# Performance work log

Hardware: AMD Instinct MI355X
Metric: run time of the kernel (lower is better)

Reference implementation:

```python
import jax, jax.numpy as jnp
from jax import lax
import numpy as np

B, MAX_FRAME, CAPLEN = 64, 40, 20
H, E, V = 512, 512, 32000


def setup_inputs() -> dict:
    key = jax.random.key(0)
    ks = jax.random.split(key, 9)
    s = 0.02
    return {
        "feature": jax.random.normal(ks[0], (B, MAX_FRAME + CAPLEN, H), dtype=jnp.float32),
        "captions": jax.random.randint(ks[1], (B, CAPLEN), 0, V),
        "embedding": jax.random.normal(ks[2], (V, E), dtype=jnp.float32) * s,
        "W_ih": jax.random.normal(ks[3], (4 * H, E + H), dtype=jnp.float32) * s,
        "W_hh": jax.random.normal(ks[4], (4 * H, H), dtype=jnp.float32) * s,
        "b_ih": jax.random.normal(ks[5], (4 * H,), dtype=jnp.float32) * s,
        "b_hh": jax.random.normal(ks[6], (4 * H,), dtype=jnp.float32) * s,
        "W_lin": jax.random.normal(ks[7], (V, H), dtype=jnp.float32) * s,
        "b_lin": jax.random.normal(ks[8], (V,), dtype=jnp.float32) * s,
    }


def _lstm_scan(xs, W_ih, W_hh, b, h0, c0):
    """xs: [T, B, D]; PyTorch gate order i, f, g, o."""
    def step(carry, x):
        h, c = carry
        gates = x @ W_ih.T + h @ W_hh.T + b  # [B, 4H]
        i, f, g, o = jnp.split(gates, 4, axis=-1)
        c = jax.nn.sigmoid(f) * c + jax.nn.sigmoid(i) * jnp.tanh(g)
        h = jax.nn.sigmoid(o) * jnp.tanh(c)
        return (h, c), h
    _, hs = lax.scan(step, (h0, c0), xs)
    return hs  # [T, B, H]


def reference(feature, captions, embedding, W_ih, W_hh, b_ih, b_hh, W_lin, b_lin):
    batch = feature.shape[0]
    caplen = captions.shape[1]
    max_frame = feature.shape[1] - caplen
    hdim = W_hh.shape[1]
    edim = embedding.shape[1]

    emb = embedding[captions]  # [B, caplen, E]
    # encoding phase: pad token (zeros) concat frame feature
    pad = jnp.zeros((batch, max_frame, edim), feature.dtype)
    enc_x = jnp.concatenate([pad, feature[:, :max_frame, :]], axis=2)  # [B, mf, E+H]
    # decoding phase: embedded word concat frame feature
    dec_x = jnp.concatenate([emb, feature[:, max_frame:, :]], axis=2)  # [B, caplen, E+H]
    xs = jnp.concatenate([enc_x, dec_x], axis=1).transpose(1, 0, 2)  # [T, B, E+H]

    h0 = jnp.zeros((batch, hdim), feature.dtype)
    c0 = jnp.zeros((batch, hdim), feature.dtype)
    hs = _lstm_scan(xs, W_ih, W_hh, b_ih + b_hh, h0, c0)  # [T, B, H]

    dec_h = hs[max_frame:].transpose(1, 0, 2)  # [B, caplen, H]
    logits = dec_h @ W_lin.T + b_lin  # [B, caplen, V]
    logits = logits[:, :-1, :]  # drop last step, as in original
    return logits.reshape(batch * (caplen - 1), -1)
```

## Files before the change

kernel.cpp:

```cpp
#include <hip/hip_runtime.h>
#include <hip/hip_bf16.h>


typedef short bf16x8 __attribute__((ext_vector_type(8)));
typedef float f32x4 __attribute__((ext_vector_type(4)));

__device__ inline short f2bf(float f) {
    unsigned u = __float_as_uint(f);
    unsigned r = (u + 0x7fffu + ((u >> 16) & 1u)) >> 16;
    return (short)r;
}
__device__ inline int4 ld8_f32_to_bf16(const float* __restrict__ g) {
    float4 a = *(const float4*)g;
    float4 b = *(const float4*)(g + 4);
    union { short s[8]; int4 v; } u;
    u.s[0] = f2bf(a.x); u.s[1] = f2bf(a.y); u.s[2] = f2bf(a.z); u.s[3] = f2bf(a.w);
    u.s[4] = f2bf(b.x); u.s[5] = f2bf(b.y); u.s[6] = f2bf(b.z); u.s[7] = f2bf(b.w);
    return u.v;
}
__device__ inline float sigf(float x) { return 1.0f / (1.0f + expf(-x)); }

__device__ inline float sig_fast(float x) {
    return __builtin_amdgcn_rcpf(1.0f + __expf(-x));
}
__device__ inline float tanh_fast(float x) {
    return 1.0f - 2.0f * __builtin_amdgcn_rcpf(1.0f + __expf(2.0f * x));
}

__device__ inline void gload_lds16(const void* g, void* l) {
    __builtin_amdgcn_global_load_lds(
        (const __attribute__((address_space(1))) void*)g,
        (__attribute__((address_space(3))) void*)l, 16, 0, 0);
}

__global__ __launch_bounds__(256) void gemm_xproj(
    const float* __restrict__ feature,
    const int*   __restrict__ captions,
    const float* __restrict__ embedding,
    const float* __restrict__ W_ih,
    const float* __restrict__ b_ih,
    const float* __restrict__ b_hh,
    float* __restrict__ Xp)
{
    __shared__ __align__(16) short Al[128 * 72];
    __shared__ __align__(16) short Bl[128 * 72];
    const int tid  = threadIdx.x;
    const int wave = tid >> 6, lane = tid & 63;
    const int quad = lane >> 4, l16 = lane & 15;
    const int m0 = blockIdx.y * 128;
    const int n0 = blockIdx.x * 128;
    const int wm = (wave >> 1) * 64, wn = (wave & 1) * 64;
    const int sr = tid >> 3;
    const int sc = (tid & 7) * 8;

    f32x4 acc[4][4] = {};

    for (int k0 = 0; k0 < 1024; k0 += 64) {
        const int j = k0 + sc;
#pragma unroll
        for (int p = 0; p < 4; ++p) {
            int r = sr + p * 32;
            int row = m0 + r;
            int t = row >> 6, b = row & 63;
            int4 val;
            if (j < 512) {
                if (t >= 40) {
                    int tok = captions[b * 20 + (t - 40)];
                    val = ld8_f32_to_bf16(&embedding[(size_t)tok * 512 + j]);
                } else {
                    val = make_int4(0, 0, 0, 0);
                }
            } else {
                val = ld8_f32_to_bf16(&feature[(size_t)(b * 60 + t) * 512 + (j - 512)]);
            }
            *(int4*)&Al[r * 72 + sc] = val;
            *(int4*)&Bl[r * 72 + sc] = ld8_f32_to_bf16(&W_ih[(size_t)(n0 + r) * 1024 + j]);
        }
        __syncthreads();
#pragma unroll
        for (int kk = 0; kk < 64; kk += 32) {
            bf16x8 af[4], bg[4];
#pragma unroll
            for (int i = 0; i < 4; ++i)
                af[i] = *(const bf16x8*)&Al[(wm + i * 16 + l16) * 72 + kk + quad * 8];
#pragma unroll
            for (int jj = 0; jj < 4; ++jj)
                bg[jj] = *(const bf16x8*)&Bl[(wn + jj * 16 + l16) * 72 + kk + quad * 8];
#pragma unroll
            for (int i = 0; i < 4; ++i)
#pragma unroll
                for (int jj = 0; jj < 4; ++jj)
                    acc[i][jj] = __builtin_amdgcn_mfma_f32_16x16x32_bf16(
                        af[i], bg[jj], acc[i][jj], 0, 0, 0);
        }
        __syncthreads();
    }

#pragma unroll
    for (int jj = 0; jj < 4; ++jj) {
        int n = n0 + wn + jj * 16 + l16;
        float bv = b_ih[n] + b_hh[n];
#pragma unroll
        for (int i = 0; i < 4; ++i) {
            int mbase = m0 + wm + i * 16 + quad * 4;
#pragma unroll
            for (int r = 0; r < 4; ++r)
                Xp[(size_t)(mbase + r) * 2048 + n] = acc[i][jj][r] + bv;
        }
    }
}

__global__ __launch_bounds__(256) void cvt_bf16(
    const float* __restrict__ src, short* __restrict__ dst, int n8)
{
    int i = blockIdx.x * 256 + threadIdx.x;
    if (i < n8)
        *(int4*)&dst[(size_t)i * 8] = ld8_f32_to_bf16(&src[(size_t)i * 8]);
}

template <bool BF16B>
__global__ __launch_bounds__(256) void gemm_out(
    const short* __restrict__ A,
    const void*  __restrict__ Wv,
    const float* __restrict__ bias,
    float* __restrict__ C,
    int M, int N, int K)
{
    __shared__ __align__(16) short Al[128 * 72];
    __shared__ __align__(16) short Bl[128 * 72];
    const int tid  = threadIdx.x;
    const int wave = tid >> 6, lane = tid & 63;
    const int quad = lane >> 4, l16 = lane & 15;
    const int m0 = blockIdx.y * 128;
    const int n0 = blockIdx.x * 128;
    const int wm = (wave >> 1) * 64, wn = (wave & 1) * 64;
    const int sr = tid >> 3;
    const int sc = (tid & 7) * 8;

    f32x4 acc[4][4] = {};

    for (int k0 = 0; k0 < K; k0 += 64) {
        if (BF16B) {
            const char* Ab = (const char*)A;
            const char* Wb = (const char*)Wv;
            char* AlB = (char*)Al;
            char* BlB = (char*)Bl;
#pragma unroll
            for (int p = 0; p < 4; ++p) {
                int row = p * 32 + wave * 8 + (lane >> 3);
                int ss  = ((lane & 7) ^ (row & 7)) << 4;
                int am  = m0 + row; am = (am < M) ? am : (M - 1);
                gload_lds16(Ab + (size_t)am * 1024 + k0 * 2 + ss,
                            AlB + p * 4096 + wave * 1024);
                gload_lds16(Wb + (size_t)(n0 + row) * 1024 + k0 * 2 + ss,
                            BlB + p * 4096 + wave * 1024);
            }
        } else {
#pragma unroll
            for (int p = 0; p < 4; ++p) {
                int r = sr + p * 32;
                int am = m0 + r;
                am = (am < M) ? am : (M - 1);
                *(int4*)&Al[r * 72 + sc] = *(const int4*)&A[(size_t)am * K + k0 + sc];
                *(int4*)&Bl[r * 72 + sc] =
                    ld8_f32_to_bf16(&((const float*)Wv)[(size_t)(n0 + r) * K + k0 + sc]);
            }
        }
        __syncthreads();
#pragma unroll
        for (int kk = 0; kk < 64; kk += 32) {
            bf16x8 af[4], bg[4];
            if (BF16B) {
                const int s_ = (kk >> 3) + quad;
#pragma unroll
                for (int i = 0; i < 4; ++i) {
                    int rw = wm + i * 16 + l16;
                    af[i] = *(const bf16x8*)&Al[rw * 64 + ((s_ ^ (rw & 7)) << 3)];
                }
#pragma unroll
                for (int jj = 0; jj < 4; ++jj) {
                    int rw = wn + jj * 16 + l16;
                    bg[jj] = *(const bf16x8*)&Bl[rw * 64 + ((s_ ^ (rw & 7)) << 3)];
                }
            } else {
#pragma unroll
                for (int i = 0; i < 4; ++i)
                    af[i] = *(const bf16x8*)&Al[(wm + i * 16 + l16) * 72 + kk + quad * 8];
#pragma unroll
                for (int jj = 0; jj < 4; ++jj)
                    bg[jj] = *(const bf16x8*)&Bl[(wn + jj * 16 + l16) * 72 + kk + quad * 8];
            }
#pragma unroll
            for (int i = 0; i < 4; ++i)
#pragma unroll
                for (int jj = 0; jj < 4; ++jj)
                    acc[i][jj] = __builtin_amdgcn_mfma_f32_16x16x32_bf16(
                        af[i], bg[jj], acc[i][jj], 0, 0, 0);
        }
        __syncthreads();
    }

#pragma unroll
    for (int jj = 0; jj < 4; ++jj) {
        int n = n0 + wn + jj * 16 + l16;
        float bv = bias[n];
#pragma unroll
        for (int i = 0; i < 4; ++i) {
            int mbase = m0 + wm + i * 16 + quad * 4;
#pragma unroll
            for (int r = 0; r < 4; ++r) {
                int m = mbase + r;
                if (m < M)
                    C[(size_t)m * N + n] = acc[i][jj][r] + bv;
            }
        }
    }
}

#define LSTM_BLOCKS 32

__global__ __launch_bounds__(256, 1) void lstm_persist(
    const float* __restrict__ Xp,
    const float* __restrict__ W_hh,
    unsigned long long* __restrict__ hbuf,
    unsigned long long* __restrict__ dec_h,
    unsigned* __restrict__ flags)
{
    __shared__ __align__(16) short Wl[64 * 512];
    __shared__ __align__(16) short Ht[4][16][16];
    const int tid  = threadIdx.x;
    const int wave = tid >> 6, lane = tid & 63;
    const int quad = lane >> 4, l16 = lane & 15;
    const int nb = blockIdx.x * 16;
    const int swz = (l16 & 7) << 3;

#pragma unroll
    for (int it = 0; it < 16; ++it) {
        int rr = (tid >> 6) + it * 4;
        int k  = (tid & 63) * 8;
        int s = rr >> 4, col = rr & 15;
        *(int4*)&Wl[(rr * 512 + k) ^ ((rr & 7) << 3)] =
            ld8_f32_to_bf16(&W_hh[(size_t)(s * 512 + nb + col) * 512 + k]);
    }
    float creg[4] = {0.f, 0.f, 0.f, 0.f};

    const int n = nb + l16;
    float xg[4][4];
#pragma unroll
    for (int r = 0; r < 4; ++r) {
        const float* xr = Xp + (size_t)(wave * 16 + quad * 4 + r) * 2048;
        xg[r][0] = xr[n];
        xg[r][1] = xr[512 + n];
        xg[r][2] = xr[1024 + n];
        xg[r][3] = xr[1536 + n];
    }
    __syncthreads();

    for (int t = 0; t < 59; ++t) {
        f32x4 acc[4] = {};
        if (t > 0) {
            const unsigned long long* hrow =
                hbuf + ((size_t)((t & 1) ^ 1) << 13)
                     + (size_t)(wave * 16 + l16) * 128 + quad * 2;
            union { unsigned long long q[2]; bf16x8 v; } hu[16];
#pragma unroll
            for (int kk = 0; kk < 16; ++kk) {
                hu[kk].q[0] = __hip_atomic_load(&hrow[kk * 8],
                                 __ATOMIC_RELAXED, __HIP_MEMORY_SCOPE_AGENT);
                hu[kk].q[1] = __hip_atomic_load(&hrow[kk * 8 + 1],
                                 __ATOMIC_RELAXED, __HIP_MEMORY_SCOPE_AGENT);
            }
            __builtin_amdgcn_sched_barrier(0);
#pragma unroll
            for (int kk = 0; kk < 16; ++kk) {
#pragma unroll
                for (int s = 0; s < 4; ++s) {
                    bf16x8 bg = *(const bf16x8*)
                        &Wl[((s * 16 + l16) * 512 + kk * 32 + quad * 8) ^ swz];
                    acc[s] = __builtin_amdgcn_mfma_f32_16x16x32_bf16(hu[kk].v, bg, acc[s], 0, 0, 0);
                }
            }
        }
#pragma unroll
        for (int r = 0; r < 4; ++r) {
            float iv = acc[0][r] + xg[r][0];
            float fv = acc[1][r] + xg[r][1];
            float gv = acc[2][r] + xg[r][2];
            float ov = acc[3][r] + xg[r][3];
            float cn = sig_fast(fv) * creg[r] + sig_fast(iv) * tanh_fast(gv);
            float hn = sig_fast(ov) * tanh_fast(cn);
            creg[r] = cn;
            Ht[wave][quad * 4 + r][l16] = f2bf(hn);
        }
        asm volatile("s_waitcnt lgkmcnt(0)" ::: "memory");
        unsigned long long* hout64 = hbuf + ((size_t)(t & 1) << 13);
        {
            int row = lane >> 2, qp = lane & 3;
            unsigned long long v = *(const unsigned long long*)&Ht[wave][row][qp * 4];
            int m = wave * 16 + row;
            __hip_atomic_store(&hout64[m * 128 + (nb >> 2) + qp], v,
                               __ATOMIC_RELAXED, __HIP_MEMORY_SCOPE_AGENT);
            if (t >= 40)
                dec_h[(size_t)(m * 19 + (t - 40)) * 128 + (nb >> 2) + qp] = v;
        }
        if (t < 58) {
            float xn_[4][4];
            const float* xt = Xp + (size_t)(t + 1) * 131072;
#pragma unroll
            for (int r = 0; r < 4; ++r) {
                const float* xr = xt + (size_t)(wave * 16 + quad * 4 + r) * 2048;
                xn_[r][0] = xr[n];
                xn_[r][1] = xr[512 + n];
                xn_[r][2] = xr[1024 + n];
                xn_[r][3] = xr[1536 + n];
            }
            __syncthreads();
            if (tid == 0)
                __hip_atomic_store(&flags[blockIdx.x], (unsigned)(t + 1),
                                   __ATOMIC_RELAXED, __HIP_MEMORY_SCOPE_AGENT);
            if (tid < LSTM_BLOCKS) {
                int guard = 0;
                while (__hip_atomic_load(&flags[tid], __ATOMIC_RELAXED,
                                         __HIP_MEMORY_SCOPE_AGENT) < (unsigned)(t + 1)
                       && guard < (1 << 16)) {
                    __builtin_amdgcn_s_sleep(1);
                    ++guard;
                }
            }
            __syncthreads();
#pragma unroll
            for (int r = 0; r < 4; ++r)
#pragma unroll
                for (int g = 0; g < 4; ++g)
                    xg[r][g] = xn_[r][g];
        }
    }
}

extern "C" void kernel_launch(void* const* d_in, const int* in_sizes, int n_in,
                              void* d_out, int out_size, void* d_ws, size_t ws_size,
                              hipStream_t stream)
{
    (void)in_sizes; (void)n_in; (void)out_size;
    const float* feature   = (const float*)d_in[0];
    const int*   captions  = (const int*)d_in[1];
    const float* embedding = (const float*)d_in[2];
    const float* W_ih      = (const float*)d_in[3];
    const float* W_hh      = (const float*)d_in[4];
    const float* b_ih      = (const float*)d_in[5];
    const float* b_hh      = (const float*)d_in[6];
    const float* W_lin     = (const float*)d_in[7];
    const float* b_lin     = (const float*)d_in[8];
    float* out = (float*)d_out;

    char* ws = (char*)d_ws;
    unsigned long long* hbuf = (unsigned long long*)(ws);
    short*    dech = (short*)(ws + 131072);
    unsigned* flags = (unsigned*)(ws + 1376256);
    short*    wbf  = (short*)(ws + 1376512);
    const bool big = ws_size >= (size_t)1376512 + 32768000;

    float* Xp = (float*)d_out;

    hipMemsetAsync(flags, 0, 256, stream);

    if (big)
        cvt_bf16<<<8000, 256, 0, stream>>>(W_lin, wbf, 2048000);

    gemm_xproj<<<dim3(16, 30), 256, 0, stream>>>(
        feature, captions, embedding, W_ih, b_ih, b_hh, Xp);

    lstm_persist<<<LSTM_BLOCKS, 256, 0, stream>>>(
        Xp, W_hh, hbuf, (unsigned long long*)dech, flags);

    if (big)
        gemm_out<true><<<dim3(250, 10), 256, 0, stream>>>(
            dech, wbf, b_lin, out, 1216, 32000, 512);
    else
        gemm_out<false><<<dim3(250, 10), 256, 0, stream>>>(
            dech, W_lin, b_lin, out, 1216, 32000, 512);
}
```

Before: 747.3 us.

## Fuse LSTM recurrence and output projection into one persistent kernel with flag waits

Merges the persistent LSTM blocks and the vocabulary projection GEMM into a single launch. The GEMM blocks spin on per-block step flags and start on their row tiles as soon as the needed decoder timesteps are published. dec_h is stored time-major with output rows remapped at store time, and Xp moves to workspace so it no longer shares the output buffer. The aim is to overlap the projection with the serial recurrence and drop a launch. The risks are spinning GEMM blocks taking CUs or memory bandwidth from the LSTM blocks, and a possible deadlock if the 32 LSTM blocks are not scheduled ahead of the waiters.

```diff
diff --git a/kernel.cpp b/kernel.cpp
--- a/kernel.cpp
+++ b/kernel.cpp
@@ -18,15 +18,12 @@
     u.s[4] = f2bf(b.x); u.s[5] = f2bf(b.y); u.s[6] = f2bf(b.z); u.s[7] = f2bf(b.w);
     return u.v;
 }
-__device__ inline float sigf(float x) { return 1.0f / (1.0f + expf(-x)); }
-
 __device__ inline float sig_fast(float x) {
     return __builtin_amdgcn_rcpf(1.0f + __expf(-x));
 }
 __device__ inline float tanh_fast(float x) {
     return 1.0f - 2.0f * __builtin_amdgcn_rcpf(1.0f + __expf(2.0f * x));
 }
-
 __device__ inline void gload_lds16(const void* g, void* l) {
     __builtin_amdgcn_global_load_lds(
         (const __attribute__((address_space(1))) void*)g,
@@ -209,9 +206,11 @@
             int mbase = m0 + wm + i * 16 + quad * 4;
 #pragma unroll
             for (int r = 0; r < 4; ++r) {
-                int m = mbase + r;
-                if (m < M)
-                    C[(size_t)m * N + n] = acc[i][jj][r] + bv;
+                int ar = mbase + r;
+                if (ar < M) {
+                    int crow = (ar & 63) * 19 + (ar >> 6);
+                    C[(size_t)crow * N + n] = acc[i][jj][r] + bv;
+                }
             }
         }
     }
@@ -219,120 +218,231 @@
 
 #define LSTM_BLOCKS 32
 
-__global__ __launch_bounds__(256, 1) void lstm_persist(
+__global__ __launch_bounds__(256, 1) void mega(
     const float* __restrict__ Xp,
     const float* __restrict__ W_hh,
     unsigned long long* __restrict__ hbuf,
     unsigned long long* __restrict__ dec_h,
-    unsigned* __restrict__ flags)
+    unsigned* __restrict__ flags,
+    const short* __restrict__ wbf,
+    const float* __restrict__ b_lin,
+    float* __restrict__ out)
 {
-    __shared__ __align__(16) short Wl[64 * 512];
-    __shared__ __align__(16) short Ht[4][16][16];
+    __shared__ __align__(16) char smem[147456];
     const int tid  = threadIdx.x;
     const int wave = tid >> 6, lane = tid & 63;
     const int quad = lane >> 4, l16 = lane & 15;
-    const int nb = blockIdx.x * 16;
-    const int swz = (l16 & 7) << 3;
-
-#pragma unroll
-    for (int it = 0; it < 16; ++it) {
-        int rr = (tid >> 6) + it * 4;
-        int k  = (tid & 63) * 8;
-        int s = rr >> 4, col = rr & 15;
-        *(int4*)&Wl[(rr * 512 + k) ^ ((rr & 7) << 3)] =
-            ld8_f32_to_bf16(&W_hh[(size_t)(s * 512 + nb + col) * 512 + k]);
-    }
-    float creg[4] = {0.f, 0.f, 0.f, 0.f};
-
-    const int n = nb + l16;
-    float xg[4][4];
-#pragma unroll
-    for (int r = 0; r < 4; ++r) {
-        const float* xr = Xp + (size_t)(wave * 16 + quad * 4 + r) * 2048;
-        xg[r][0] = xr[n];
-        xg[r][1] = xr[512 + n];
-        xg[r][2] = xr[1024 + n];
-        xg[r][3] = xr[1536 + n];
+
+    if (blockIdx.x < LSTM_BLOCKS) {
+        short* Wl  = (short*)smem;
+        short* Htb = (short*)(smem + 65536);
+        const int nb = blockIdx.x * 16;
+        const int swz = (l16 & 7) << 3;
+
+#pragma unroll
+        for (int it = 0; it < 16; ++it) {
+            int rr = (tid >> 6) + it * 4;
+            int k  = (tid & 63) * 8;
+            int s = rr >> 4, col = rr & 15;
+            *(int4*)&Wl[(rr * 512 + k) ^ ((rr & 7) << 3)] =
+                ld8_f32_to_bf16(&W_hh[(size_t)(s * 512 + nb + col) * 512 + k]);
+        }
+        float creg[4] = {0.f, 0.f, 0.f, 0.f};
+
+        const int n = nb + l16;
+        float xg[4][4];
+#pragma unroll
+        for (int r = 0; r < 4; ++r) {
+            const float* xr = Xp + (size_t)(wave * 16 + quad * 4 + r) * 2048;
+            xg[r][0] = xr[n];
+            xg[r][1] = xr[512 + n];
+            xg[r][2] = xr[1024 + n];
+            xg[r][3] = xr[1536 + n];
+        }
+        __syncthreads();
+
+        for (int t = 0; t < 59; ++t) {
+            f32x4 acc[4] = {};
+            if (t > 0) {
+                const unsigned long long* hrow =
+                    hbuf + ((size_t)((t & 1) ^ 1) << 13)
+                         + (size_t)(wave * 16 + l16) * 128 + quad * 2;
+                union { unsigned long long q[2]; bf16x8 v; } hu[16];
+#pragma unroll
+                for (int kk = 0; kk < 16; ++kk) {
+                    hu[kk].q[0] = __hip_atomic_load(&hrow[kk * 8],
+                                     __ATOMIC_RELAXED, __HIP_MEMORY_SCOPE_AGENT);
+                    hu[kk].q[1] = __hip_atomic_load(&hrow[kk * 8 + 1],
+                                     __ATOMIC_RELAXED, __HIP_MEMORY_SCOPE_AGENT);
+                }
+                __builtin_amdgcn_sched_barrier(0);
+#pragma unroll
+                for (int kk = 0; kk < 16; ++kk) {
+#pragma unroll
+                    for (int s = 0; s < 4; ++s) {
+                        bf16x8 bg = *(const bf16x8*)
+                            &Wl[((s * 16 + l16) * 512 + kk * 32 + quad * 8) ^ swz];
+                        acc[s] = __builtin_amdgcn_mfma_f32_16x16x32_bf16(
+                            hu[kk].v, bg, acc[s], 0, 0, 0);
+                    }
+                }
+            }
+#pragma unroll
+            for (int r = 0; r < 4; ++r) {
+                float iv = acc[0][r] + xg[r][0];
+                float fv = acc[1][r] + xg[r][1];
+                float gv = acc[2][r] + xg[r][2];
+                float ov = acc[3][r] + xg[r][3];
+                float cn = sig_fast(fv) * creg[r] + sig_fast(iv) * tanh_fast(gv);
+                float hn = sig_fast(ov) * tanh_fast(cn);
+                creg[r] = cn;
+                Htb[(wave << 8) + ((quad * 4 + r) << 4) + l16] = f2bf(hn);
+            }
+            asm volatile("s_waitcnt lgkmcnt(0)" ::: "memory");
+            unsigned long long* hout64 = hbuf + ((size_t)(t & 1) << 13);
+            {
+                int row = lane >> 2, qp = lane & 3;
+                unsigned long long v =
+                    *(const unsigned long long*)&Htb[(wave << 8) + (row << 4) + qp * 4];
+                int m = wave * 16 + row;
+                __hip_atomic_store(&hout64[m * 128 + (nb >> 2) + qp], v,
+                                   __ATOMIC_RELAXED, __HIP_MEMORY_SCOPE_AGENT);
+                if (t >= 40)
+                    __hip_atomic_store(
+                        &dec_h[(size_t)((t - 40) * 64 + m) * 128 + (nb >> 2) + qp], v,
+                        __ATOMIC_RELAXED, __HIP_MEMORY_SCOPE_AGENT);
+            }
+            if (t < 58) {
+                float xn_[4][4];
+                const float* xt = Xp + (size_t)(t + 1) * 131072;
+#pragma unroll
+                for (int r = 0; r < 4; ++r) {
+                    const float* xr = xt + (size_t)(wave * 16 + quad * 4 + r) * 2048;
+                    xn_[r][0] = xr[n];
+                    xn_[r][1] = xr[512 + n];
+                    xn_[r][2] = xr[1024 + n];
+                    xn_[r][3] = xr[1536 + n];
+                }
+                __syncthreads();
+                if (tid == 0)
+                    __hip_atomic_store(&flags[blockIdx.x], (unsigned)(t + 1),
+                                       __ATOMIC_RELAXED, __HIP_MEMORY_SCOPE_AGENT);
+                if (tid < LSTM_BLOCKS) {
+                    int guard = 0;
+                    while (__hip_atomic_load(&flags[tid], __ATOMIC_RELAXED,
+                                             __HIP_MEMORY_SCOPE_AGENT) < (unsigned)(t + 1)
+                           && guard < (1 << 16)) {
+                        __builtin_amdgcn_s_sleep(1);
+                        ++guard;
+                    }
+                }
+                __syncthreads();
+#pragma unroll
+                for (int r = 0; r < 4; ++r)
+#pragma unroll
+                    for (int g = 0; g < 4; ++g)
+                        xg[r][g] = xn_[r][g];
+            }
+        }
+        __syncthreads();
+        if (tid == 0)
+            __hip_atomic_store(&flags[blockIdx.x], 59u,
+                               __ATOMIC_RELAXED, __HIP_MEMORY_SCOPE_AGENT);
+        return;
+    }
+
+    short* As = (short*)smem;
+    short* Bt = (short*)(smem + 131072);
+    const int cid = blockIdx.x - LSTM_BLOCKS;
+    const int n0 = (cid % 250) * 128;
+    const int mt = cid / 250;
+    const int m0 = mt * 128;
+    const int M = 1216;
+    const int wm = (wave >> 1) * 64, wn = (wave & 1) * 64;
+    int maxa = m0 + 127; maxa = (maxa < M - 1) ? maxa : (M - 1);
+    const unsigned v = 41u + (unsigned)(maxa >> 6);
+
+    if (tid < LSTM_BLOCKS) {
+        int guard = 0;
+        while (__hip_atomic_load(&flags[tid], __ATOMIC_RELAXED,
+                                 __HIP_MEMORY_SCOPE_AGENT) < v
+               && guard < (1 << 14)) {
+            __builtin_amdgcn_s_sleep(32);
+            ++guard;
+        }
     }
     __syncthreads();
 
-    for (int t = 0; t < 59; ++t) {
-        f32x4 acc[4] = {};
-        if (t > 0) {
-            const unsigned long long* hrow =
-                hbuf + ((size_t)((t & 1) ^ 1) << 13)
-                     + (size_t)(wave * 16 + l16) * 128 + quad * 2;
-            union { unsigned long long q[2]; bf16x8 v; } hu[16];
-#pragma unroll
-            for (int kk = 0; kk < 16; ++kk) {
-                hu[kk].q[0] = __hip_atomic_load(&hrow[kk * 8],
-                                 __ATOMIC_RELAXED, __HIP_MEMORY_SCOPE_AGENT);
-                hu[kk].q[1] = __hip_atomic_load(&hrow[kk * 8 + 1],
-                                 __ATOMIC_RELAXED, __HIP_MEMORY_SCOPE_AGENT);
-            }
-            __builtin_amdgcn_sched_barrier(0);
-#pragma unroll
-            for (int kk = 0; kk < 16; ++kk) {
-#pragma unroll
-                for (int s = 0; s < 4; ++s) {
-                    bf16x8 bg = *(const bf16x8*)
-                        &Wl[((s * 16 + l16) * 512 + kk * 32 + quad * 8) ^ swz];
-                    acc[s] = __builtin_amdgcn_mfma_f32_16x16x32_bf16(hu[kk].v, bg, acc[s], 0, 0, 0);
-                }
-            }
-        }
-#pragma unroll
-        for (int r = 0; r < 4; ++r) {
-            float iv = acc[0][r] + xg[r][0];
-            float fv = acc[1][r] + xg[r][1];
-            float gv = acc[2][r] + xg[r][2];
-            float ov = acc[3][r] + xg[r][3];
-            float cn = sig_fast(fv) * creg[r] + sig_fast(iv) * tanh_fast(gv);
-            float hn = sig_fast(ov) * tanh_fast(cn);
-            creg[r] = cn;
-            Ht[wave][quad * 4 + r][l16] = f2bf(hn);
-        }
-        asm volatile("s_waitcnt lgkmcnt(0)" ::: "memory");
-        unsigned long long* hout64 = hbuf + ((size_t)(t & 1) << 13);
-        {
-            int row = lane >> 2, qp = lane & 3;
-            unsigned long long v = *(const unsigned long long*)&Ht[wave][row][qp * 4];
-            int m = wave * 16 + row;
-            __hip_atomic_store(&hout64[m * 128 + (nb >> 2) + qp], v,
-                               __ATOMIC_RELAXED, __HIP_MEMORY_SCOPE_AGENT);
-            if (t >= 40)
-                dec_h[(size_t)(m * 19 + (t - 40)) * 128 + (nb >> 2) + qp] = v;
-        }
-        if (t < 58) {
-            float xn_[4][4];
-            const float* xt = Xp + (size_t)(t + 1) * 131072;
+    {
+        int row = tid >> 1, half = tid & 1;
+        int ar = m0 + row; ar = (ar < M) ? ar : (M - 1);
+        const unsigned long long* g = dec_h + (size_t)ar * 128 + half * 64;
+        const int cbase = half * 256;
+#pragma unroll
+        for (int j = 0; j < 32; ++j) {
+            union { unsigned long long q[2]; int4 v4; } u;
+            u.q[0] = __hip_atomic_load(&g[j * 2],
+                         __ATOMIC_RELAXED, __HIP_MEMORY_SCOPE_AGENT);
+            u.q[1] = __hip_atomic_load(&g[j * 2 + 1],
+                         __ATOMIC_RELAXED, __HIP_MEMORY_SCOPE_AGENT);
+            int off = (row * 512 + cbase + j * 8) ^ ((row & 7) << 3);
+            *(int4*)&As[off] = u.v4;
+        }
+    }
+
+    f32x4 acc[4][4] = {};
+    const char* Wb = (const char*)wbf;
+    char* BtB = (char*)Bt;
+    const int swzA = (l16 & 7) << 3;
+
+    for (int k0 = 0; k0 < 512; k0 += 64) {
+#pragma unroll
+        for (int p = 0; p < 4; ++p) {
+            int row = p * 32 + wave * 8 + (lane >> 3);
+            int ss  = ((lane & 7) ^ (row & 7)) << 4;
+            gload_lds16(Wb + (size_t)(n0 + row) * 1024 + k0 * 2 + ss,
+                        BtB + p * 4096 + wave * 1024);
+        }
+        __syncthreads();
+#pragma unroll
+        for (int kk = 0; kk < 64; kk += 32) {
+            bf16x8 af[4], bg[4];
+            const int s_ = (kk >> 3) + quad;
+#pragma unroll
+            for (int i = 0; i < 4; ++i) {
+                int rw = wm + i * 16 + l16;
+                af[i] = *(const bf16x8*)&As[(rw * 512 + k0 + kk + quad * 8) ^ swzA];
+            }
+#pragma unroll
+            for (int jj = 0; jj < 4; ++jj) {
+                int rw = wn + jj * 16 + l16;
+                bg[jj] = *(const bf16x8*)&Bt[rw * 64 + ((s_ ^ (rw & 7)) << 3)];
+            }
+#pragma unroll
+            for (int i = 0; i < 4; ++i)
+#pragma unroll
+                for (int jj = 0; jj < 4; ++jj)
+                    acc[i][jj] = __builtin_amdgcn_mfma_f32_16x16x32_bf16(
+                        af[i], bg[jj], acc[i][jj], 0, 0, 0);
+        }
+        __syncthreads();
+    }
+
+#pragma unroll
+    for (int jj = 0; jj < 4; ++jj) {
+        int n = n0 + wn + jj * 16 + l16;
+        float bv = b_lin[n];
+#pragma unroll
+        for (int i = 0; i < 4; ++i) {
+            int mbase = m0 + wm + i * 16 + quad * 4;
 #pragma unroll
             for (int r = 0; r < 4; ++r) {
-                const float* xr = xt + (size_t)(wave * 16 + quad * 4 + r) * 2048;
-                xn_[r][0] = xr[n];
-                xn_[r][1] = xr[512 + n];
-                xn_[r][2] = xr[1024 + n];
-                xn_[r][3] = xr[1536 + n];
-            }
-            __syncthreads();
-            if (tid == 0)
-                __hip_atomic_store(&flags[blockIdx.x], (unsigned)(t + 1),
-                                   __ATOMIC_RELAXED, __HIP_MEMORY_SCOPE_AGENT);
-            if (tid < LSTM_BLOCKS) {
-                int guard = 0;
-                while (__hip_atomic_load(&flags[tid], __ATOMIC_RELAXED,
-                                         __HIP_MEMORY_SCOPE_AGENT) < (unsigned)(t + 1)
-                       && guard < (1 << 16)) {
-                    __builtin_amdgcn_s_sleep(1);
-                    ++guard;
-                }
-            }
-            __syncthreads();
-#pragma unroll
-            for (int r = 0; r < 4; ++r)
-#pragma unroll
-                for (int g = 0; g < 4; ++g)
-                    xg[r][g] = xn_[r][g];
+                int ar = mbase + r;
+                if (ar < M) {
+                    int crow = (ar & 63) * 19 + (ar >> 6);
+                    out[(size_t)crow * 32000 + n] = acc[i][jj][r] + bv;
+                }
+            }
         }
     }
 }
@@ -355,12 +465,14 @@
 
     char* ws = (char*)d_ws;
     unsigned long long* hbuf = (unsigned long long*)(ws);
-    short*    dech = (short*)(ws + 131072);
+    unsigned long long* dech = (unsigned long long*)(ws + 131072);
     unsigned* flags = (unsigned*)(ws + 1376256);
-    short*    wbf  = (short*)(ws + 1376512);
-    const bool big = ws_size >= (size_t)1376512 + 32768000;
-
-    float* Xp = (float*)d_out;
+    short*    wbf   = (short*)(ws + 1376512);
+    float*    xpws  = (float*)(ws + 34144512);
+    const bool big  = ws_size >= (size_t)34144512;
+    const bool bigx = ws_size >= (size_t)34144512 + 31457280;
+
+    float* Xp = bigx ? xpws : (float*)d_out;
 
     hipMemsetAsync(flags, 0, 256, stream);
 
@@ -370,13 +482,17 @@
     gemm_xproj<<<dim3(16, 30), 256, 0, stream>>>(
         feature, captions, embedding, W_ih, b_ih, b_hh, Xp);
 
-    lstm_persist<<<LSTM_BLOCKS, 256, 0, stream>>>(
-        Xp, W_hh, hbuf, (unsigned long long*)dech, flags);
-
-    if (big)
-        gemm_out<true><<<dim3(250, 10), 256, 0, stream>>>(
-            dech, wbf, b_lin, out, 1216, 32000, 512);
-    else
-        gemm_out<false><<<dim3(250, 10), 256, 0, stream>>>(
-            dech, W_lin, b_lin, out, 1216, 32000, 512);
-}
+    if (bigx) {
+        mega<<<dim3(LSTM_BLOCKS + 2500), 256, 0, stream>>>(
+            Xp, W_hh, hbuf, dech, flags, wbf, b_lin, out);
+    } else {
+        mega<<<dim3(LSTM_BLOCKS), 256, 0, stream>>>(
+            Xp, W_hh, hbuf, dech, flags, (const short*)nullptr, b_lin, out);
+        if (big)
+            gemm_out<true><<<dim3(250, 10), 256, 0, stream>>>(
+                (const short*)dech, wbf, b_lin, out, 1216, 32000, 512);
+        else
+            gemm_out<false><<<dim3(250, 10), 256, 0, stream>>>(
+                (const short*)dech, W_lin, b_lin, out, 1216, 32000, 512);
+    }
+}
```

New measurement: 884.0 us. 18.3% more time.
